# Performance work log

Measured on AMD Instinct MI355X. Metric: run time of the kernel, lower is better.

Reference implementation:

```python
import jax, jax.numpy as jnp
import numpy as np

N_USERS, N_ITEMS = 40000, 60000
N = N_USERS + N_ITEMS
N_EDGES = 600000
IN_DIM, HID, OUT = 128, 256, 256


def setup_inputs() -> dict:
    key = jax.random.key(0)
    ks = jax.random.split(key, 8)
    return {
        "user_feat": jax.random.normal(ks[0], (N_USERS, IN_DIM), jnp.float32),
        "item_feat": jax.random.normal(ks[1], (N_ITEMS, IN_DIM), jnp.float32),
        "edge_rows": jax.random.randint(ks[2], (N_EDGES,), 0, N, jnp.int32),
        "edge_cols": jax.random.randint(ks[3], (N_EDGES,), 0, N, jnp.int32),
        "edge_vals": jax.random.uniform(ks[4], (N_EDGES,), jnp.float32),
        "W0": jax.random.normal(ks[5], (IN_DIM, HID), jnp.float32) * (1.0 / np.sqrt(IN_DIM)),
        "b0": jnp.zeros((HID,), jnp.float32),
        "Wres0": jax.random.normal(ks[6], (IN_DIM, HID), jnp.float32) * (1.0 / np.sqrt(IN_DIM)),
        "W1": jax.random.normal(ks[7], (HID, OUT), jnp.float32) * (1.0 / np.sqrt(HID)),
        "b1": jnp.zeros((OUT,), jnp.float32),
    }


def reference(user_feat, item_feat, edge_rows, edge_cols, edge_vals, W0, b0, Wres0, W1, b1):
    n_users = user_feat.shape[0]
    n_total = n_users + item_feat.shape[0]

    def spmm(x):  # sparse adjacency @ dense features via gather + segment-sum
        return jax.ops.segment_sum(edge_vals[:, None] * x[edge_cols], edge_rows,
                                   num_segments=n_total)

    # Layer 0: fc -> SpMM -> linear residual -> relu (norm=None, dropout eval no-op)
    x = jnp.concatenate([user_feat @ W0 + b0, item_feat @ W0 + b0])  # [N, HID]
    h = spmm(x)
    res = jnp.concatenate([user_feat, item_feat]) @ Wres0  # in_dim != out_dim -> Linear residual
    h = jax.nn.relu(h + res)

    # Layer 1 (last, encoding=False): fc -> SpMM, no residual/norm/activation
    x = h @ W1 + b1
    h = spmm(x)

    return h[:n_users], h[n_users:]
```

## Files before the change

### kernel.cpp

```cpp
#include <hip/hip_runtime.h>

#define N_USERS 40000
#define N_ITEMS 60000
#define N_TOTAL 100000
#define M_PAD   100032
#define NEDGES  600000
#define IN_DIM  128
#define HID     256

typedef short  bf16x8 __attribute__((ext_vector_type(8)));
typedef float  f32x4  __attribute__((ext_vector_type(4)));
typedef unsigned short ushort4v __attribute__((ext_vector_type(4)));
typedef unsigned short ushort8v __attribute__((ext_vector_type(8)));

__device__ __forceinline__ unsigned short f2bf(float f) {
    unsigned u = __builtin_bit_cast(unsigned, f);
    unsigned r = (u + 0x7FFFu + ((u >> 16) & 1u)) >> 16;
    return (unsigned short)r;
}
__device__ __forceinline__ float bf2f(unsigned short b) {
    unsigned u = ((unsigned)b) << 16;
    return __builtin_bit_cast(float, u);
}

__global__ __launch_bounds__(256) void prep_feats(const float* __restrict__ uf,
                                                  const float* __restrict__ itf,
                                                  unsigned short* __restrict__ outp) {
    const long i8 = (long)(blockIdx.x * 256 + threadIdx.x) * 8;
    if (i8 >= (long)N_TOTAL * IN_DIM) return;
    const long uend = (long)N_USERS * IN_DIM;
    const float4* src = (i8 < uend) ? (const float4*)(uf + i8)
                                    : (const float4*)(itf + (i8 - uend));
    float4 a = src[0], b = src[1];
    ushort8v o;
    o[0] = f2bf(a.x); o[1] = f2bf(a.y); o[2] = f2bf(a.z); o[3] = f2bf(a.w);
    o[4] = f2bf(b.x); o[5] = f2bf(b.y); o[6] = f2bf(b.z); o[7] = f2bf(b.w);
    *(ushort8v*)(outp + i8) = o;
}

__global__ __launch_bounds__(256) void prep_weights(const float* __restrict__ W0,
                                                    const float* __restrict__ Wres0,
                                                    const float* __restrict__ W1,
                                                    unsigned short* __restrict__ Wcat_t,
                                                    unsigned short* __restrict__ W1_t) {
    const int id = blockIdx.x * 256 + threadIdx.x;
    if (id < 512 * IN_DIM) {
        const int n = id >> 7, k = id & 127;
        const float v = (n < HID) ? W0[(size_t)k * HID + n]
                                  : Wres0[(size_t)k * HID + (n - HID)];
        Wcat_t[id] = f2bf(v);
    } else {
        const int id2 = id - 512 * IN_DIM;
        const int n = id2 >> 8, k = id2 & 255;
        W1_t[id2] = f2bf(W1[(size_t)k * HID + n]);
    }
}

template <int K, int EPI>
__global__ __launch_bounds__(256) void mfma_gemm(const unsigned short* __restrict__ A,
                                                 const unsigned short* __restrict__ Bt,
                                                 const float* __restrict__ bias,
                                                 unsigned short* __restrict__ out0,
                                                 unsigned short* __restrict__ out1) {
    __shared__ unsigned short As[64 * 32];
    __shared__ unsigned short Bs[64 * 32];
    const int t  = threadIdx.x;
    const int m0 = blockIdx.x * 64;
    const int n0 = blockIdx.y * 64;
    const int w  = t >> 6, l = t & 63;
    const int fr = l & 15, fb = l >> 4;

    f32x4 acc[4] = {};
    const unsigned short* Ap = A  + (size_t)(m0 + (t >> 2)) * K + (t & 3) * 8;
    const unsigned short* Bp = Bt + (size_t)(n0 + (t >> 2)) * K + (t & 3) * 8;

    for (int kk = 0; kk < K; kk += 32) {
        const ushort8v av = *(const ushort8v*)(Ap + kk);
        const ushort8v bv = *(const ushort8v*)(Bp + kk);
        __syncthreads();
        *(ushort8v*)(As + t * 8) = av;
        *(ushort8v*)(Bs + t * 8) = bv;
        __syncthreads();
        const bf16x8 af = *(const bf16x8*)(As + (16 * w + fr) * 32 + fb * 8);
        #pragma unroll
        for (int nt = 0; nt < 4; ++nt) {
            const bf16x8 bfr = *(const bf16x8*)(Bs + (nt * 16 + fr) * 32 + fb * 8);
            acc[nt] = __builtin_amdgcn_mfma_f32_16x16x32_bf16(af, bfr, acc[nt], 0, 0, 0);
        }
    }

    #pragma unroll
    for (int nt = 0; nt < 4; ++nt) {
        const int col = n0 + nt * 16 + fr;
        #pragma unroll
        for (int r = 0; r < 4; ++r) {
            const int row = m0 + 16 * w + fb * 4 + r;
            if (row >= N_TOTAL) continue;
            const float v = acc[nt][r];
            if (EPI == 0) {
                out0[(size_t)row * HID + col] = f2bf(v + bias[col]);
            } else {
                if (col < HID) out0[(size_t)row * HID + col] = f2bf(v + bias[col]);
                else           out1[(size_t)row * HID + (col - HID)] = f2bf(v);
            }
        }
    }
}

__global__ __launch_bounds__(256) void edge_histogram(const int* __restrict__ rows,
                                                      int* __restrict__ cnt) {
    int e = blockIdx.x * 256 + threadIdx.x;
    if (e < NEDGES) atomicAdd(&cnt[rows[e]], 1);
}

#define SCAN_B 1024
__global__ __launch_bounds__(SCAN_B) void scan_blocks(const int* __restrict__ cnt,
                                                      int* __restrict__ row_ptr,
                                                      int* __restrict__ bsums) {
    __shared__ int s[SCAN_B];
    const int gid = blockIdx.x * SCAN_B + threadIdx.x;
    const int v = (gid < N_TOTAL) ? cnt[gid] : 0;
    s[threadIdx.x] = v;
    __syncthreads();
    for (int off = 1; off < SCAN_B; off <<= 1) {
        int tv = (threadIdx.x >= off) ? s[threadIdx.x - off] : 0;
        __syncthreads();
        s[threadIdx.x] += tv;
        __syncthreads();
    }
    if (gid < N_TOTAL) row_ptr[gid] = s[threadIdx.x] - v;
    if (threadIdx.x == SCAN_B - 1) bsums[blockIdx.x] = s[threadIdx.x];
}

__global__ __launch_bounds__(128) void scan_sums(int* __restrict__ bsums, int nb) {
    __shared__ int s[128];
    const int v = (threadIdx.x < nb) ? bsums[threadIdx.x] : 0;
    s[threadIdx.x] = v;
    __syncthreads();
    for (int off = 1; off < 128; off <<= 1) {
        int tv = (threadIdx.x >= off) ? s[threadIdx.x - off] : 0;
        __syncthreads();
        s[threadIdx.x] += tv;
        __syncthreads();
    }
    if (threadIdx.x < nb) bsums[threadIdx.x] = s[threadIdx.x] - v;
}

__global__ __launch_bounds__(SCAN_B) void scan_apply(int* __restrict__ row_ptr,
                                                     const int* __restrict__ bsums,
                                                     int* __restrict__ next) {
    const int gid = blockIdx.x * SCAN_B + threadIdx.x;
    if (gid < N_TOTAL) {
        const int p = row_ptr[gid] + bsums[blockIdx.x];
        row_ptr[gid] = p;
        next[gid] = p;
    }
    if (gid == 0) row_ptr[N_TOTAL] = NEDGES;
}

__global__ __launch_bounds__(256) void csr_fill(const int* __restrict__ rows,
                                                const int* __restrict__ cols,
                                                const float* __restrict__ vals,
                                                int* __restrict__ next,
                                                int* __restrict__ ccol,
                                                float* __restrict__ cval) {
    int e = blockIdx.x * 256 + threadIdx.x;
    if (e >= NEDGES) return;
    const int slot = atomicAdd(&next[rows[e]], 1);
    ccol[slot] = cols[e];
    cval[slot] = vals[e];
}

template <bool FUSE>
__global__ __launch_bounds__(256) void spmm_bf16(const int* __restrict__ row_ptr,
                                                 const int* __restrict__ ccol,
                                                 const float* __restrict__ cval,
                                                 const unsigned short* __restrict__ X,
                                                 unsigned short* __restrict__ Ybf,
                                                 float* __restrict__ Yf) {
    const int wid  = (blockIdx.x * 256 + threadIdx.x) >> 6;
    const int lane = threadIdx.x & 63;
    if (wid >= N_TOTAL) return;
    const int beg = row_ptr[wid], end = row_ptr[wid + 1];

    float a0 = 0.f, a1 = 0.f, a2 = 0.f, a3 = 0.f;
    int e = beg;
    for (; e + 1 < end; e += 2) {
        const int   c0 = ccol[e],     c1 = ccol[e + 1];
        const float v0 = cval[e],     v1 = cval[e + 1];
        const ushort4v x0 = *(const ushort4v*)(X + (size_t)c0 * HID + lane * 4);
        const ushort4v x1 = *(const ushort4v*)(X + (size_t)c1 * HID + lane * 4);
        a0 = fmaf(v0, bf2f(x0[0]), a0); a1 = fmaf(v0, bf2f(x0[1]), a1);
        a2 = fmaf(v0, bf2f(x0[2]), a2); a3 = fmaf(v0, bf2f(x0[3]), a3);
        a0 = fmaf(v1, bf2f(x1[0]), a0); a1 = fmaf(v1, bf2f(x1[1]), a1);
        a2 = fmaf(v1, bf2f(x1[2]), a2); a3 = fmaf(v1, bf2f(x1[3]), a3);
    }
    if (e < end) {
        const int   c0 = ccol[e];
        const float v0 = cval[e];
        const ushort4v x0 = *(const ushort4v*)(X + (size_t)c0 * HID + lane * 4);
        a0 = fmaf(v0, bf2f(x0[0]), a0); a1 = fmaf(v0, bf2f(x0[1]), a1);
        a2 = fmaf(v0, bf2f(x0[2]), a2); a3 = fmaf(v0, bf2f(x0[3]), a3);
    }

    if (FUSE) {
        unsigned short* yp = Ybf + (size_t)wid * HID + lane * 4;
        const ushort4v rv = *(const ushort4v*)yp;
        a0 = fmaxf(a0 + bf2f(rv[0]), 0.f);
        a1 = fmaxf(a1 + bf2f(rv[1]), 0.f);
        a2 = fmaxf(a2 + bf2f(rv[2]), 0.f);
        a3 = fmaxf(a3 + bf2f(rv[3]), 0.f);
        ushort4v o; o[0] = f2bf(a0); o[1] = f2bf(a1); o[2] = f2bf(a2); o[3] = f2bf(a3);
        *(ushort4v*)yp = o;
    } else {
        f32x4 o = {a0, a1, a2, a3};
        *(f32x4*)(Yf + (size_t)wid * HID + lane * 4) = o;
    }
}

extern "C" void kernel_launch(void* const* d_in, const int* in_sizes, int n_in,
                              void* d_out, int out_size, void* d_ws, size_t ws_size,
                              hipStream_t stream) {
    const float* user_feat = (const float*)d_in[0];
    const float* item_feat = (const float*)d_in[1];
    const int*   edge_rows = (const int*)d_in[2];
    const int*   edge_cols = (const int*)d_in[3];
    const float* edge_vals = (const float*)d_in[4];
    const float* W0    = (const float*)d_in[5];
    const float* b0    = (const float*)d_in[6];
    const float* Wres0 = (const float*)d_in[7];
    const float* W1    = (const float*)d_in[8];
    const float* b1    = (const float*)d_in[9];
    float* out = (float*)d_out;

    char* ws = (char*)d_ws;
    auto take = [&](size_t bytes) { char* p = ws; ws += (bytes + 255) & ~(size_t)255; return p; };
    unsigned short* x      = (unsigned short*)take((size_t)M_PAD * HID * 2);
    unsigned short* h      = (unsigned short*)take((size_t)M_PAD * HID * 2);
    unsigned short* feats  = (unsigned short*)take((size_t)M_PAD * IN_DIM * 2);
    unsigned short* Wcat_t = (unsigned short*)take(512 * IN_DIM * 2);
    unsigned short* W1_t   = (unsigned short*)take(HID * HID * 2);
    int*   row_ptr = (int*)take((N_TOTAL + 1) * 4);
    int*   cnt     = (int*)take(N_TOTAL * 4);
    int*   nxt     = (int*)take(N_TOTAL * 4);
    int*   bsums   = (int*)take(128 * 4);
    int*   ccol    = (int*)take(NEDGES * 4);
    float* cval    = (float*)take(NEDGES * 4);

    const dim3 blk(256);
    const int nscan = (N_TOTAL + SCAN_B - 1) / SCAN_B;

    prep_feats<<<(N_TOTAL * IN_DIM / 8 + 255) / 256, blk, 0, stream>>>(user_feat, item_feat, feats);
    prep_weights<<<(512 * IN_DIM + HID * HID) / 256, blk, 0, stream>>>(W0, Wres0, W1, Wcat_t, W1_t);

    hipMemsetAsync(cnt, 0, N_TOTAL * 4, stream);
    edge_histogram<<<(NEDGES + 255) / 256, blk, 0, stream>>>(edge_rows, cnt);
    scan_blocks<<<nscan, SCAN_B, 0, stream>>>(cnt, row_ptr, bsums);
    scan_sums<<<1, 128, 0, stream>>>(bsums, nscan);
    scan_apply<<<nscan, SCAN_B, 0, stream>>>(row_ptr, bsums, nxt);
    csr_fill<<<(NEDGES + 255) / 256, blk, 0, stream>>>(edge_rows, edge_cols, edge_vals,
                                                       nxt, ccol, cval);

    mfma_gemm<IN_DIM, 1><<<dim3(M_PAD / 64, 8), blk, 0, stream>>>(feats, Wcat_t, b0, x, h);

    const int spmm_blocks = (N_TOTAL * 64 + 255) / 256;
    spmm_bf16<true><<<spmm_blocks, blk, 0, stream>>>(row_ptr, ccol, cval, x, h, nullptr);

    mfma_gemm<HID, 0><<<dim3(M_PAD / 64, 4), blk, 0, stream>>>(h, W1_t, b1, x, nullptr);

    spmm_bf16<false><<<spmm_blocks, blk, 0, stream>>>(row_ptr, ccol, cval, x, nullptr, out);
}
```

Before: 460.3 us.

## Restructure GEMM to 64x256 tiles with direct-to-LDS loads; pack CSR col/val pairs

The GEMM now gives each block a 64x256 output tile. The whole A panel stays resident in swizzled LDS, and B is double-buffered and staged with global_load_lds, so A is read once per block rather than once per 64-column tile. Each wave computes a 32x128 sub-tile with more MFMAs per LDS read. Separately, CSR column indices and values are packed into a single int2 array so SpMM fetches both with one load. The cost is larger LDS use, which can lower occupancy, plus fewer blocks in the y dimension.

```diff
diff --git a/kernel.cpp b/kernel.cpp
--- a/kernel.cpp
+++ b/kernel.cpp
@@ -21,6 +21,12 @@
 __device__ __forceinline__ float bf2f(unsigned short b) {
     unsigned u = ((unsigned)b) << 16;
     return __builtin_bit_cast(float, u);
+}
+
+__device__ __forceinline__ void gload_lds16(const void* g, void* l) {
+    __builtin_amdgcn_global_load_lds(
+        (const __attribute__((address_space(1))) unsigned int*)g,
+        (__attribute__((address_space(3))) unsigned int*)l, 16, 0, 0);
 }
 
 __global__ __launch_bounds__(256) void prep_feats(const float* __restrict__ uf,
@@ -56,52 +62,84 @@
     }
 }
 
+template <int K>
+__device__ __forceinline__ void stageB(const unsigned short* __restrict__ Bg,
+                                       char* bs, int kk, int t) {
+    #pragma unroll
+    for (int i = 0; i < 4; ++i) {
+        const int L = (i * 256 + t) * 16;
+        const int n = L >> 6;
+        const int q = (L >> 4) & 3;
+        gload_lds16((const char*)(Bg + (size_t)n * K + kk + q * 8), bs + L);
+    }
+}
+
 template <int K, int EPI>
-__global__ __launch_bounds__(256) void mfma_gemm(const unsigned short* __restrict__ A,
-                                                 const unsigned short* __restrict__ Bt,
-                                                 const float* __restrict__ bias,
-                                                 unsigned short* __restrict__ out0,
-                                                 unsigned short* __restrict__ out1) {
-    __shared__ unsigned short As[64 * 32];
-    __shared__ unsigned short Bs[64 * 32];
+__global__ __launch_bounds__(256) void mfma_gemm2(const unsigned short* __restrict__ A,
+                                                  const unsigned short* __restrict__ Bt,
+                                                  const float* __restrict__ bias,
+                                                  unsigned short* __restrict__ out0,
+                                                  unsigned short* __restrict__ out1) {
+    constexpr int NK    = K / 32;
+    constexpr int SHIFT = (K == 256) ? 9 : 8;
+    __shared__ unsigned short As[64 * K];
+    __shared__ unsigned short Bs[2][256 * 32];
+
     const int t  = threadIdx.x;
-    const int m0 = blockIdx.x * 64;
-    const int n0 = blockIdx.y * 64;
     const int w  = t >> 6, l = t & 63;
     const int fr = l & 15, fb = l >> 4;
-
-    f32x4 acc[4] = {};
-    const unsigned short* Ap = A  + (size_t)(m0 + (t >> 2)) * K + (t & 3) * 8;
-    const unsigned short* Bp = Bt + (size_t)(n0 + (t >> 2)) * K + (t & 3) * 8;
-
-    for (int kk = 0; kk < K; kk += 32) {
-        const ushort8v av = *(const ushort8v*)(Ap + kk);
-        const ushort8v bv = *(const ushort8v*)(Bp + kk);
-        __syncthreads();
-        *(ushort8v*)(As + t * 8) = av;
-        *(ushort8v*)(Bs + t * 8) = bv;
-        __syncthreads();
-        const bf16x8 af = *(const bf16x8*)(As + (16 * w + fr) * 32 + fb * 8);
+    const int wr = w >> 1, wc = w & 1;
+    const int m0 = blockIdx.x * 64;
+    const int gy = blockIdx.y;
+
+    const char* Ag = (const char*)(A + (size_t)m0 * K);
+    constexpr int ACALLS = (64 * K * 2) / (16 * 256);
+    #pragma unroll
+    for (int i = 0; i < ACALLS; ++i) {
+        const int L = (i * 256 + t) * 16;
+        const int U = L ^ (((L >> SHIFT) & 7) << 4);
+        gload_lds16(Ag + U, (char*)As + L);
+    }
+    const unsigned short* Bg = Bt + (size_t)gy * 256 * K;
+    stageB<K>(Bg, (char*)Bs[0], 0, t);
+    __syncthreads();
+
+    f32x4 acc[2][8] = {};
+    for (int kt = 0; kt < NK; ++kt) {
+        if (kt + 1 < NK) stageB<K>(Bg, (char*)Bs[(kt + 1) & 1], (kt + 1) * 32, t);
+
+        const char* as_base = (const char*)As;
+        const char* bs_base = (const char*)Bs[kt & 1];
+        bf16x8 af[2];
         #pragma unroll
-        for (int nt = 0; nt < 4; ++nt) {
-            const bf16x8 bfr = *(const bf16x8*)(Bs + (nt * 16 + fr) * 32 + fb * 8);
-            acc[nt] = __builtin_amdgcn_mfma_f32_16x16x32_bf16(af, bfr, acc[nt], 0, 0, 0);
+        for (int rb = 0; rb < 2; ++rb) {
+            const int row = wr * 32 + rb * 16 + fr;
+            const int Sa = ((row * K + kt * 32 + fb * 8) * 2) ^ ((fr & 7) << 4);
+            af[rb] = *(const bf16x8*)(as_base + Sa);
         }
-    }
-
+        #pragma unroll
+        for (int nt = 0; nt < 8; ++nt) {
+            const int Sb = ((wc * 128 + nt * 16 + fr) * 32 + fb * 8) * 2;
+            const bf16x8 bfr = *(const bf16x8*)(bs_base + Sb);
+            acc[0][nt] = __builtin_amdgcn_mfma_f32_16x16x32_bf16(af[0], bfr, acc[0][nt], 0, 0, 0);
+            acc[1][nt] = __builtin_amdgcn_mfma_f32_16x16x32_bf16(af[1], bfr, acc[1][nt], 0, 0, 0);
+        }
+        __syncthreads();
+    }
+
+    const bool use1 = (EPI == 1) && (gy == 1);
+    unsigned short* outp = use1 ? out1 : out0;
     #pragma unroll
-    for (int nt = 0; nt < 4; ++nt) {
-        const int col = n0 + nt * 16 + fr;
+    for (int rb = 0; rb < 2; ++rb) {
         #pragma unroll
-        for (int r = 0; r < 4; ++r) {
-            const int row = m0 + 16 * w + fb * 4 + r;
-            if (row >= N_TOTAL) continue;
-            const float v = acc[nt][r];
-            if (EPI == 0) {
-                out0[(size_t)row * HID + col] = f2bf(v + bias[col]);
-            } else {
-                if (col < HID) out0[(size_t)row * HID + col] = f2bf(v + bias[col]);
-                else           out1[(size_t)row * HID + (col - HID)] = f2bf(v);
+        for (int nt = 0; nt < 8; ++nt) {
+            const int col = wc * 128 + nt * 16 + fr;
+            const float bv = use1 ? 0.f : bias[col];
+            #pragma unroll
+            for (int j = 0; j < 4; ++j) {
+                const int row = m0 + wr * 32 + rb * 16 + fb * 4 + j;
+                if (row < N_TOTAL)
+                    outp[(size_t)row * HID + col] = f2bf(acc[rb][nt][j] + bv);
             }
         }
     }
@@ -162,19 +200,19 @@
                                                 const int* __restrict__ cols,
                                                 const float* __restrict__ vals,
                                                 int* __restrict__ next,
-                                                int* __restrict__ ccol,
-                                                float* __restrict__ cval) {
+                                                int2* __restrict__ cvp) {
     int e = blockIdx.x * 256 + threadIdx.x;
     if (e >= NEDGES) return;
     const int slot = atomicAdd(&next[rows[e]], 1);
-    ccol[slot] = cols[e];
-    cval[slot] = vals[e];
+    int2 p;
+    p.x = cols[e];
+    p.y = __builtin_bit_cast(int, vals[e]);
+    cvp[slot] = p;
 }
 
 template <bool FUSE>
 __global__ __launch_bounds__(256) void spmm_bf16(const int* __restrict__ row_ptr,
-                                                 const int* __restrict__ ccol,
-                                                 const float* __restrict__ cval,
+                                                 const int2* __restrict__ cvp,
                                                  const unsigned short* __restrict__ X,
                                                  unsigned short* __restrict__ Ybf,
                                                  float* __restrict__ Yf) {
@@ -186,19 +224,20 @@
     float a0 = 0.f, a1 = 0.f, a2 = 0.f, a3 = 0.f;
     int e = beg;
     for (; e + 1 < end; e += 2) {
-        const int   c0 = ccol[e],     c1 = ccol[e + 1];
-        const float v0 = cval[e],     v1 = cval[e + 1];
-        const ushort4v x0 = *(const ushort4v*)(X + (size_t)c0 * HID + lane * 4);
-        const ushort4v x1 = *(const ushort4v*)(X + (size_t)c1 * HID + lane * 4);
+        const int2 p0 = cvp[e], p1 = cvp[e + 1];
+        const float v0 = __builtin_bit_cast(float, p0.y);
+        const float v1 = __builtin_bit_cast(float, p1.y);
+        const ushort4v x0 = *(const ushort4v*)(X + (size_t)p0.x * HID + lane * 4);
+        const ushort4v x1 = *(const ushort4v*)(X + (size_t)p1.x * HID + lane * 4);
         a0 = fmaf(v0, bf2f(x0[0]), a0); a1 = fmaf(v0, bf2f(x0[1]), a1);
         a2 = fmaf(v0, bf2f(x0[2]), a2); a3 = fmaf(v0, bf2f(x0[3]), a3);
         a0 = fmaf(v1, bf2f(x1[0]), a0); a1 = fmaf(v1, bf2f(x1[1]), a1);
         a2 = fmaf(v1, bf2f(x1[2]), a2); a3 = fmaf(v1, bf2f(x1[3]), a3);
     }
     if (e < end) {
-        const int   c0 = ccol[e];
-        const float v0 = cval[e];
-        const ushort4v x0 = *(const ushort4v*)(X + (size_t)c0 * HID + lane * 4);
+        const int2 p0 = cvp[e];
+        const float v0 = __builtin_bit_cast(float, p0.y);
+        const ushort4v x0 = *(const ushort4v*)(X + (size_t)p0.x * HID + lane * 4);
         a0 = fmaf(v0, bf2f(x0[0]), a0); a1 = fmaf(v0, bf2f(x0[1]), a1);
         a2 = fmaf(v0, bf2f(x0[2]), a2); a3 = fmaf(v0, bf2f(x0[3]), a3);
     }
@@ -244,8 +283,7 @@
     int*   cnt     = (int*)take(N_TOTAL * 4);
     int*   nxt     = (int*)take(N_TOTAL * 4);
     int*   bsums   = (int*)take(128 * 4);
-    int*   ccol    = (int*)take(NEDGES * 4);
-    float* cval    = (float*)take(NEDGES * 4);
+    int2*  cvp     = (int2*)take((size_t)NEDGES * 8);
 
     const dim3 blk(256);
     const int nscan = (N_TOTAL + SCAN_B - 1) / SCAN_B;
@@ -259,14 +297,14 @@
     scan_sums<<<1, 128, 0, stream>>>(bsums, nscan);
     scan_apply<<<nscan, SCAN_B, 0, stream>>>(row_ptr, bsums, nxt);
     csr_fill<<<(NEDGES + 255) / 256, blk, 0, stream>>>(edge_rows, edge_cols, edge_vals,
-                                                       nxt, ccol, cval);
-
-    mfma_gemm<IN_DIM, 1><<<dim3(M_PAD / 64, 8), blk, 0, stream>>>(feats, Wcat_t, b0, x, h);
+                                                       nxt, cvp);
+
+    mfma_gemm2<IN_DIM, 1><<<dim3(M_PAD / 64, 2), blk, 0, stream>>>(feats, Wcat_t, b0, x, h);
 
     const int spmm_blocks = (N_TOTAL * 64 + 255) / 256;
-    spmm_bf16<true><<<spmm_blocks, blk, 0, stream>>>(row_ptr, ccol, cval, x, h, nullptr);
-
-    mfma_gemm<HID, 0><<<dim3(M_PAD / 64, 4), blk, 0, stream>>>(h, W1_t, b1, x, nullptr);
-
-    spmm_bf16<false><<<spmm_blocks, blk, 0, stream>>>(row_ptr, ccol, cval, x, nullptr, out);
-}
+    spmm_bf16<true><<<spmm_blocks, blk, 0, stream>>>(row_ptr, cvp, x, h, nullptr);
+
+    mfma_gemm2<HID, 0><<<dim3(M_PAD / 64, 1), blk, 0, stream>>>(h, W1_t, b1, x, nullptr);
+
+    spmm_bf16<false><<<spmm_blocks, blk, 0, stream>>>(row_ptr, cvp, x, nullptr, out);
+}
```

Result: no change. 458.5 us (-0.4%).
